# Kernel optimization log

Hardware: AMD Instinct MI355X
Metric: run time of the kernel (lower is better)

The kernel has to match this reference:

```python
import jax, jax.numpy as jnp
import numpy as np

ATTWSIZE = 64  # sliding window length (matches init_kwargs attwsize)


def setup_inputs() -> dict:
    key = jax.random.key(0)
    k1, k2, k3 = jax.random.split(key, 3)
    B, T, D, A = 32, 4096, 256, 128
    x = jax.random.normal(k1, (B, T, D), dtype=jnp.float32)
    Wp = jax.random.normal(k2, (A, D), dtype=jnp.float32) / np.sqrt(D).astype(np.float32)
    bp = jnp.zeros((A,), dtype=jnp.float32)
    Wg = jax.random.normal(k3, (1, A), dtype=jnp.float32) / np.sqrt(A).astype(np.float32)
    return {"x": x, "Wp": Wp, "bp": bp, "Wg": Wg}


def _windowed_sum(v, w):
    # causal sliding-window sum over axis=1: sum(v[:, max(t-w+1,0):t+1, :])
    # single-pass cumsum formulation: cs[t] - cs[t-w]
    cs = jnp.cumsum(v, axis=1)
    T = v.shape[1]
    shifted = jnp.pad(cs, ((0, 0), (w, 0), (0, 0)))[:, :T, :]
    return cs - shifted


def reference(x, Wp, bp, Wg):
    # proj = tanh(Linear(dimio->dimatt)(x))
    proj = jnp.tanh(jnp.einsum('btd,ad->bta', x, Wp) + bp)
    # gvec = sigmoid(Linear(dimatt->1, no bias)(proj))  -> [B, T, 1]
    g = jax.nn.sigmoid(jnp.einsum('bta,oa->bto', proj, Wg))
    wx = g * x  # gated input [B, T, D]
    num = _windowed_sum(wx, ATTWSIZE)         # [B, T, D]
    den = _windowed_sum(g, ATTWSIZE)          # [B, T, 1] broadcasts over D
    return num / den
```

## Files before the change

kernel.cpp:

```cpp
#include <hip/hip_runtime.h>

#define TT 4096
#define DD 256
#define AA 128
#define WIN 64

typedef short bf16x8 __attribute__((ext_vector_type(8)));
typedef float f32x4 __attribute__((ext_vector_type(4)));
typedef unsigned int u32x4 __attribute__((ext_vector_type(4)));

__device__ __forceinline__ unsigned short f2bf(float f) {
    unsigned int u = __builtin_bit_cast(unsigned int, f);
    u += 0x7FFFu + ((u >> 16) & 1u);
    return (unsigned short)(u >> 16);
}

__device__ __forceinline__ unsigned int cvt_pk_bf16(float lo, float hi) {
    unsigned int r;
    asm("v_cvt_pk_bf16_f32 %0, %1, %2" : "=v"(r) : "v"(lo), "v"(hi));
    return r;
}

__global__ __launch_bounds__(256) void prep_wp(const float* __restrict__ Wp,
                                               unsigned short* __restrict__ wpb) {
    int i = blockIdx.x * 256 + threadIdx.x;
    wpb[i] = f2bf(Wp[i]);
}

#define SROWS 32
#define TC    512
#define NU    ((TC + WIN) / SROWS)
#define NCHK  (TT / TC)

__global__ __launch_bounds__(256, 1) void fused_kernel(
        const float* __restrict__ x, const unsigned short* __restrict__ wpb,
        const float* __restrict__ bp, const float* __restrict__ Wg,
        float* __restrict__ out) {
    __shared__ __align__(16) float xs[4][SROWS * DD];
    __shared__ float gbuf[4][SROWS];
    __shared__ float psum[4][SROWS];
    const int tid  = threadIdx.x;
    const int lane = tid & 63;
    const int wave = tid >> 6;
    const int quad = lane >> 4;
    const int nrow = lane & 15;
    const int sw   = nrow & 7;
    const int b     = blockIdx.x >> 3;
    const int chunk = blockIdx.x & (NCHK - 1);
    const long t0   = (long)chunk * TC;
    const float* xb = x   + (size_t)b * TT * DD;
    float*       ob = out + (size_t)b * TT * DD;

    bf16x8 bfrag[2][8];
    float bpv[2], wgv[2];
#pragma unroll
    for (int nt = 0; nt < 2; ++nt) {
        int n = wave * 32 + nt * 16 + nrow;
        bpv[nt] = bp[n];
        wgv[nt] = Wg[n];
#pragma unroll
        for (int k0 = 0; k0 < 8; ++k0)
            bfrag[nt][k0] = *reinterpret_cast<const bf16x8*>(
                wpb + n * DD + k0 * 32 + quad * 8);
    }

    auto stage = [&](int u) {
        const int nb = u & 3;
        const long r0 = t0 - WIN + (long)u * SROWS;
#pragma unroll
        for (int j = 0; j < 8; ++j) {
            int r = wave * 8 + j;
            long row = r0 + r;
            row = row < 0 ? 0 : row;
            const float* gp = xb + row * DD + ((lane ^ (r & 7)) << 2);
            __builtin_amdgcn_global_load_lds(
                (const __attribute__((address_space(1))) void*)gp,
                (__attribute__((address_space(3))) void*)&xs[nb][r * DD],
                16, 0, 0);
        }
    };

    float S = 0.f, Sg = 0.f;

    stage(0);
    asm volatile("s_waitcnt vmcnt(0)" ::: "memory");
    __builtin_amdgcn_sched_barrier(0);
    __builtin_amdgcn_s_barrier();
    __builtin_amdgcn_sched_barrier(0);

    for (int u = 0; u < NU; ++u) {
        if (u + 1 < NU) stage(u + 1);

        const float* buf = xs[u & 3];
        f32x4 acc[2][2];
#pragma unroll
        for (int mt = 0; mt < 2; ++mt)
#pragma unroll
            for (int nt = 0; nt < 2; ++nt)
                acc[mt][nt] = (f32x4){0.f, 0.f, 0.f, 0.f};
#pragma unroll
        for (int k0 = 0; k0 < 8; ++k0) {
#pragma unroll
            for (int mt = 0; mt < 2; ++mt) {
                const float* rowp = buf + (mt * 16 + nrow) * DD;
                const int gidx = quad * 2 + k0 * 8;
                float4 f0 = *reinterpret_cast<const float4*>(rowp + (((gidx)     ^ sw) << 2));
                float4 f1 = *reinterpret_cast<const float4*>(rowp + (((gidx + 1) ^ sw) << 2));
                u32x4 w;
                w.x = cvt_pk_bf16(f0.x, f0.y);
                w.y = cvt_pk_bf16(f0.z, f0.w);
                w.z = cvt_pk_bf16(f1.x, f1.y);
                w.w = cvt_pk_bf16(f1.z, f1.w);
                bf16x8 af = __builtin_bit_cast(bf16x8, w);
                acc[mt][0] = __builtin_amdgcn_mfma_f32_16x16x32_bf16(af, bfrag[0][k0], acc[mt][0], 0, 0, 0);
                acc[mt][1] = __builtin_amdgcn_mfma_f32_16x16x32_bf16(af, bfrag[1][k0], acc[mt][1], 0, 0, 0);
            }
        }
        float p[2][4];
#pragma unroll
        for (int mt = 0; mt < 2; ++mt)
#pragma unroll
            for (int r = 0; r < 4; ++r) p[mt][r] = 0.f;
#pragma unroll
        for (int nt = 0; nt < 2; ++nt) {
#pragma unroll
            for (int mt = 0; mt < 2; ++mt) {
#pragma unroll
                for (int r = 0; r < 4; ++r) {
                    float pre = acc[mt][nt][r] + bpv[nt];
                    float e  = __expf(2.0f * pre);
                    float th = 1.0f - 2.0f * __builtin_amdgcn_rcpf(e + 1.0f);
                    p[mt][r] += th * wgv[nt];
                }
            }
        }
#pragma unroll
        for (int off = 1; off <= 8; off <<= 1)
#pragma unroll
            for (int mt = 0; mt < 2; ++mt)
#pragma unroll
                for (int r = 0; r < 4; ++r)
                    p[mt][r] += __shfl_xor(p[mt][r], off, 64);
        if (nrow == 0) {
#pragma unroll
            for (int mt = 0; mt < 2; ++mt)
#pragma unroll
                for (int r = 0; r < 4; ++r)
                    psum[wave][mt * 16 + quad * 4 + r] = p[mt][r];
        }

        asm volatile("s_waitcnt lgkmcnt(0)" ::: "memory");
        __builtin_amdgcn_sched_barrier(0);
        __builtin_amdgcn_s_barrier();
        __builtin_amdgcn_sched_barrier(0);

        if (tid < SROWS) {
            float ssum = psum[0][tid] + psum[1][tid] + psum[2][tid] + psum[3][tid];
            float gg = __builtin_amdgcn_rcpf(1.0f + __expf(-ssum));
            long row = t0 - WIN + (long)u * SROWS + tid;
            gbuf[u & 3][tid] = (row < 0) ? 0.f : gg;
        }
        asm volatile("s_waitcnt lgkmcnt(0)" ::: "memory");
        __builtin_amdgcn_sched_barrier(0);
        __builtin_amdgcn_s_barrier();
        __builtin_amdgcn_sched_barrier(0);

        if (u >= 2) {
            const int v  = u - 2;
            const int bn = u & 3, bo = v & 3;
            const float* fn = xs[bn];
            const float* fo = xs[bo];
            const long tbase = t0 + (long)v * SROWS;
#pragma unroll 8
            for (int tt = 0; tt < SROWS; ++tt) {
                int off = tt * DD + ((((tid >> 2) ^ (tt & 7)) << 2) | (tid & 3));
                float gnew = gbuf[bn][tt];
                float gold = gbuf[bo][tt];
                S  += gnew * fn[off] - gold * fo[off];
                Sg += gnew - gold;
                ob[(tbase + tt) * DD + tid] = S * __builtin_amdgcn_rcpf(Sg);
            }
        } else {
            const int bn = u & 3;
            const float* fn = xs[bn];
#pragma unroll 8
            for (int tt = 0; tt < SROWS; ++tt) {
                int off = tt * DD + ((((tid >> 2) ^ (tt & 7)) << 2) | (tid & 3));
                float gnew = gbuf[bn][tt];
                S  += gnew * fn[off];
                Sg += gnew;
            }
        }

        asm volatile("s_waitcnt vmcnt(0)" ::: "memory");
        __builtin_amdgcn_sched_barrier(0);
        __builtin_amdgcn_s_barrier();
        __builtin_amdgcn_sched_barrier(0);
    }
}

extern "C" void kernel_launch(void* const* d_in, const int* in_sizes, int n_in,
                              void* d_out, int out_size, void* d_ws, size_t ws_size,
                              hipStream_t stream) {
    const float* x  = (const float*)d_in[0];
    const float* Wp = (const float*)d_in[1];
    const float* bp = (const float*)d_in[2];
    const float* Wg = (const float*)d_in[3];
    float* out = (float*)d_out;

    unsigned short* wpb = (unsigned short*)d_ws;

    prep_wp<<<AA * DD / 256, 256, 0, stream>>>(Wp, wpb);
    fused_kernel<<<32 * NCHK, 256, 0, stream>>>(x, wpb, bp, Wg, out);
}
```

Baseline: 266.3 us.

## Drop LDS staging of x, read directly from global/L2, halve chunk size

Removes the async global-to-LDS staging ring buffer of x. The MFMA projection now loads A fragments straight from global memory, and the windowed-sum loop re-reads the new and old rows of x from global, relying on L2 and cache hits. Chunk length drops from 512 to 256 rows and launch bounds allow two blocks per CU, giving twice as many blocks and more occupancy now that LDS use is small. The cost is that x is read from memory several times per chunk, including the WIN-row halo, which is now a larger share of each shorter chunk. This bets on cache reuse to make up for losing explicit prefetch overlap and one barrier per step.

```diff
diff --git a/kernel.cpp b/kernel.cpp
--- a/kernel.cpp
+++ b/kernel.cpp
@@ -28,15 +28,14 @@
 }
 
 #define SROWS 32
-#define TC    512
+#define TC    256
 #define NU    ((TC + WIN) / SROWS)
 #define NCHK  (TT / TC)
 
-__global__ __launch_bounds__(256, 1) void fused_kernel(
+__global__ __launch_bounds__(256, 2) void fused_kernel(
         const float* __restrict__ x, const unsigned short* __restrict__ wpb,
         const float* __restrict__ bp, const float* __restrict__ Wg,
         float* __restrict__ out) {
-    __shared__ __align__(16) float xs[4][SROWS * DD];
     __shared__ float gbuf[4][SROWS];
     __shared__ float psum[4][SROWS];
     const int tid  = threadIdx.x;
@@ -44,8 +43,7 @@
     const int wave = tid >> 6;
     const int quad = lane >> 4;
     const int nrow = lane & 15;
-    const int sw   = nrow & 7;
-    const int b     = blockIdx.x >> 3;
+    const int b     = blockIdx.x >> 4;
     const int chunk = blockIdx.x & (NCHK - 1);
     const long t0   = (long)chunk * TC;
     const float* xb = x   + (size_t)b * TT * DD;
@@ -64,58 +62,50 @@
                 wpb + n * DD + k0 * 32 + quad * 8);
     }
 
-    auto stage = [&](int u) {
-        const int nb = u & 3;
-        const long r0 = t0 - WIN + (long)u * SROWS;
-#pragma unroll
-        for (int j = 0; j < 8; ++j) {
-            int r = wave * 8 + j;
-            long row = r0 + r;
-            row = row < 0 ? 0 : row;
-            const float* gp = xb + row * DD + ((lane ^ (r & 7)) << 2);
-            __builtin_amdgcn_global_load_lds(
-                (const __attribute__((address_space(1))) void*)gp,
-                (__attribute__((address_space(3))) void*)&xs[nb][r * DD],
-                16, 0, 0);
-        }
-    };
-
     float S = 0.f, Sg = 0.f;
 
-    stage(0);
-    asm volatile("s_waitcnt vmcnt(0)" ::: "memory");
-    __builtin_amdgcn_sched_barrier(0);
-    __builtin_amdgcn_s_barrier();
-    __builtin_amdgcn_sched_barrier(0);
-
     for (int u = 0; u < NU; ++u) {
-        if (u + 1 < NU) stage(u + 1);
-
-        const float* buf = xs[u & 3];
+        const long rbase = t0 - WIN + (long)u * SROWS;
+
+        long R0 = rbase + nrow;
+        long R1 = rbase + 16 + nrow;
+        if (rbase < 0) {
+            R0 = R0 < 0 ? 0 : R0;
+            R1 = R1 < 0 ? 0 : R1;
+        }
+        const float* rp0 = xb + R0 * DD + quad * 8;
+        const float* rp1 = xb + R1 * DD + quad * 8;
+
         f32x4 acc[2][2];
 #pragma unroll
         for (int mt = 0; mt < 2; ++mt)
 #pragma unroll
             for (int nt = 0; nt < 2; ++nt)
                 acc[mt][nt] = (f32x4){0.f, 0.f, 0.f, 0.f};
+
 #pragma unroll
         for (int k0 = 0; k0 < 8; ++k0) {
-#pragma unroll
-            for (int mt = 0; mt < 2; ++mt) {
-                const float* rowp = buf + (mt * 16 + nrow) * DD;
-                const int gidx = quad * 2 + k0 * 8;
-                float4 f0 = *reinterpret_cast<const float4*>(rowp + (((gidx)     ^ sw) << 2));
-                float4 f1 = *reinterpret_cast<const float4*>(rowp + (((gidx + 1) ^ sw) << 2));
-                u32x4 w;
-                w.x = cvt_pk_bf16(f0.x, f0.y);
-                w.y = cvt_pk_bf16(f0.z, f0.w);
-                w.z = cvt_pk_bf16(f1.x, f1.y);
-                w.w = cvt_pk_bf16(f1.z, f1.w);
-                bf16x8 af = __builtin_bit_cast(bf16x8, w);
-                acc[mt][0] = __builtin_amdgcn_mfma_f32_16x16x32_bf16(af, bfrag[0][k0], acc[mt][0], 0, 0, 0);
-                acc[mt][1] = __builtin_amdgcn_mfma_f32_16x16x32_bf16(af, bfrag[1][k0], acc[mt][1], 0, 0, 0);
-            }
-        }
+            float4 a0 = *reinterpret_cast<const float4*>(rp0 + k0 * 32);
+            float4 a1 = *reinterpret_cast<const float4*>(rp0 + k0 * 32 + 4);
+            float4 c0 = *reinterpret_cast<const float4*>(rp1 + k0 * 32);
+            float4 c1 = *reinterpret_cast<const float4*>(rp1 + k0 * 32 + 4);
+            u32x4 w0, w1;
+            w0.x = cvt_pk_bf16(a0.x, a0.y);
+            w0.y = cvt_pk_bf16(a0.z, a0.w);
+            w0.z = cvt_pk_bf16(a1.x, a1.y);
+            w0.w = cvt_pk_bf16(a1.z, a1.w);
+            w1.x = cvt_pk_bf16(c0.x, c0.y);
+            w1.y = cvt_pk_bf16(c0.z, c0.w);
+            w1.z = cvt_pk_bf16(c1.x, c1.y);
+            w1.w = cvt_pk_bf16(c1.z, c1.w);
+            bf16x8 af0 = __builtin_bit_cast(bf16x8, w0);
+            bf16x8 af1 = __builtin_bit_cast(bf16x8, w1);
+            acc[0][0] = __builtin_amdgcn_mfma_f32_16x16x32_bf16(af0, bfrag[0][k0], acc[0][0], 0, 0, 0);
+            acc[0][1] = __builtin_amdgcn_mfma_f32_16x16x32_bf16(af0, bfrag[1][k0], acc[0][1], 0, 0, 0);
+            acc[1][0] = __builtin_amdgcn_mfma_f32_16x16x32_bf16(af1, bfrag[0][k0], acc[1][0], 0, 0, 0);
+            acc[1][1] = __builtin_amdgcn_mfma_f32_16x16x32_bf16(af1, bfrag[1][k0], acc[1][1], 0, 0, 0);
+        }
+
         float p[2][4];
 #pragma unroll
         for (int mt = 0; mt < 2; ++mt)
@@ -157,8 +147,7 @@
         if (tid < SROWS) {
             float ssum = psum[0][tid] + psum[1][tid] + psum[2][tid] + psum[3][tid];
             float gg = __builtin_amdgcn_rcpf(1.0f + __expf(-ssum));
-            long row = t0 - WIN + (long)u * SROWS + tid;
-            gbuf[u & 3][tid] = (row < 0) ? 0.f : gg;
+            gbuf[u & 3][tid] = (rbase + tid < 0) ? 0.f : gg;
         }
         asm volatile("s_waitcnt lgkmcnt(0)" ::: "memory");
         __builtin_amdgcn_sched_barrier(0);
@@ -166,36 +155,33 @@
         __builtin_amdgcn_sched_barrier(0);
 
         if (u >= 2) {
-            const int v  = u - 2;
-            const int bn = u & 3, bo = v & 3;
-            const float* fn = xs[bn];
-            const float* fo = xs[bo];
-            const long tbase = t0 + (long)v * SROWS;
-#pragma unroll 8
+            const float* gn = gbuf[u & 3];
+            const float* go = gbuf[(u + 2) & 3];
+            const long tb = t0 + (long)(u - 2) * SROWS;
+#pragma unroll 16
             for (int tt = 0; tt < SROWS; ++tt) {
-                int off = tt * DD + ((((tid >> 2) ^ (tt & 7)) << 2) | (tid & 3));
-                float gnew = gbuf[bn][tt];
-                float gold = gbuf[bo][tt];
-                S  += gnew * fn[off] - gold * fo[off];
+                long tn = tb + tt;
+                long to = tn - WIN;
+                to = to < 0 ? 0 : to;
+                float gnew = gn[tt];
+                float gold = go[tt];
+                float xn = xb[tn * DD + tid];
+                float xo = xb[to * DD + tid];
+                S  += gnew * xn - gold * xo;
                 Sg += gnew - gold;
-                ob[(tbase + tt) * DD + tid] = S * __builtin_amdgcn_rcpf(Sg);
+                ob[tn * DD + tid] = S * __builtin_amdgcn_rcpf(Sg);
             }
         } else {
-            const int bn = u & 3;
-            const float* fn = xs[bn];
-#pragma unroll 8
+            const float* gn = gbuf[u & 3];
+#pragma unroll 16
             for (int tt = 0; tt < SROWS; ++tt) {
-                int off = tt * DD + ((((tid >> 2) ^ (tt & 7)) << 2) | (tid & 3));
-                float gnew = gbuf[bn][tt];
-                S  += gnew * fn[off];
+                long rn = rbase + tt;
+                rn = rn < 0 ? 0 : rn;
+                float gnew = gn[tt];
+                S  += gnew * xb[rn * DD + tid];
                 Sg += gnew;
             }
         }
-
-        asm volatile("s_waitcnt vmcnt(0)" ::: "memory");
-        __builtin_amdgcn_sched_barrier(0);
-        __builtin_amdgcn_s_barrier();
-        __builtin_amdgcn_sched_barrier(0);
     }
 }
 
```

Measured after the change: 404.1 us. 1.52x slower.

## Halve chunk size, double-buffer LDS, and read scan inputs from global memory

Applied to the files above, without the earlier changes.

Chunk length drops from 512 to 256, giving twice as many blocks, and the LDS staging shrinks from 4 to 2 buffers so two blocks can share a CU (launch bounds 256,2). The windowed-scan stage now lags the gate computation by one step and re-reads x rows straight from global/L2 instead of keeping older tiles in LDS. One barrier per iteration is removed and vmcnt(8) lets the next tile's loads stay in flight. The cost is extra global reads for the new and old rows, plus more warmup overhead because each shorter chunk still recomputes the 64-row halo.

```diff
diff --git a/kernel.cpp b/kernel.cpp
--- a/kernel.cpp
+++ b/kernel.cpp
@@ -28,15 +28,15 @@
 }
 
 #define SROWS 32
-#define TC    512
+#define TC    256
 #define NU    ((TC + WIN) / SROWS)
 #define NCHK  (TT / TC)
 
-__global__ __launch_bounds__(256, 1) void fused_kernel(
+__global__ __launch_bounds__(256, 2) void fused_kernel(
         const float* __restrict__ x, const unsigned short* __restrict__ wpb,
         const float* __restrict__ bp, const float* __restrict__ Wg,
         float* __restrict__ out) {
-    __shared__ __align__(16) float xs[4][SROWS * DD];
+    __shared__ __align__(16) float xs[2][SROWS * DD];
     __shared__ float gbuf[4][SROWS];
     __shared__ float psum[4][SROWS];
     const int tid  = threadIdx.x;
@@ -45,7 +45,7 @@
     const int quad = lane >> 4;
     const int nrow = lane & 15;
     const int sw   = nrow & 7;
-    const int b     = blockIdx.x >> 3;
+    const int b     = blockIdx.x >> 4;
     const int chunk = blockIdx.x & (NCHK - 1);
     const long t0   = (long)chunk * TC;
     const float* xb = x   + (size_t)b * TT * DD;
@@ -64,9 +64,9 @@
                 wpb + n * DD + k0 * 32 + quad * 8);
     }
 
-    auto stage = [&](int u) {
-        const int nb = u & 3;
-        const long r0 = t0 - WIN + (long)u * SROWS;
+    auto stage = [&](int su) {
+        const int nb = su & 1;
+        const long r0 = t0 - WIN + (long)su * SROWS;
 #pragma unroll
         for (int j = 0; j < 8; ++j) {
             int r = wave * 8 + j;
@@ -83,70 +83,74 @@
     float S = 0.f, Sg = 0.f;
 
     stage(0);
-    asm volatile("s_waitcnt vmcnt(0)" ::: "memory");
-    __builtin_amdgcn_sched_barrier(0);
-    __builtin_amdgcn_s_barrier();
-    __builtin_amdgcn_sched_barrier(0);
-
-    for (int u = 0; u < NU; ++u) {
+
+    for (int u = 0; u <= NU; ++u) {
         if (u + 1 < NU) stage(u + 1);
 
-        const float* buf = xs[u & 3];
-        f32x4 acc[2][2];
-#pragma unroll
-        for (int mt = 0; mt < 2; ++mt)
-#pragma unroll
-            for (int nt = 0; nt < 2; ++nt)
-                acc[mt][nt] = (f32x4){0.f, 0.f, 0.f, 0.f};
-#pragma unroll
-        for (int k0 = 0; k0 < 8; ++k0) {
-#pragma unroll
-            for (int mt = 0; mt < 2; ++mt) {
-                const float* rowp = buf + (mt * 16 + nrow) * DD;
-                const int gidx = quad * 2 + k0 * 8;
-                float4 f0 = *reinterpret_cast<const float4*>(rowp + (((gidx)     ^ sw) << 2));
-                float4 f1 = *reinterpret_cast<const float4*>(rowp + (((gidx + 1) ^ sw) << 2));
-                u32x4 w;
-                w.x = cvt_pk_bf16(f0.x, f0.y);
-                w.y = cvt_pk_bf16(f0.z, f0.w);
-                w.z = cvt_pk_bf16(f1.x, f1.y);
-                w.w = cvt_pk_bf16(f1.z, f1.w);
-                bf16x8 af = __builtin_bit_cast(bf16x8, w);
-                acc[mt][0] = __builtin_amdgcn_mfma_f32_16x16x32_bf16(af, bfrag[0][k0], acc[mt][0], 0, 0, 0);
-                acc[mt][1] = __builtin_amdgcn_mfma_f32_16x16x32_bf16(af, bfrag[1][k0], acc[mt][1], 0, 0, 0);
-            }
-        }
-        float p[2][4];
-#pragma unroll
-        for (int mt = 0; mt < 2; ++mt)
-#pragma unroll
-            for (int r = 0; r < 4; ++r) p[mt][r] = 0.f;
-#pragma unroll
-        for (int nt = 0; nt < 2; ++nt) {
-#pragma unroll
-            for (int mt = 0; mt < 2; ++mt) {
-#pragma unroll
-                for (int r = 0; r < 4; ++r) {
-                    float pre = acc[mt][nt][r] + bpv[nt];
-                    float e  = __expf(2.0f * pre);
-                    float th = 1.0f - 2.0f * __builtin_amdgcn_rcpf(e + 1.0f);
-                    p[mt][r] += th * wgv[nt];
-                }
-            }
-        }
-#pragma unroll
-        for (int off = 1; off <= 8; off <<= 1)
+        if (u + 1 < NU) asm volatile("s_waitcnt vmcnt(8) lgkmcnt(0)" ::: "memory");
+        else            asm volatile("s_waitcnt vmcnt(0) lgkmcnt(0)" ::: "memory");
+        __builtin_amdgcn_sched_barrier(0);
+        __builtin_amdgcn_s_barrier();
+        __builtin_amdgcn_sched_barrier(0);
+
+        if (u < NU) {
+            const float* buf = xs[u & 1];
+            f32x4 acc[2][2];
 #pragma unroll
             for (int mt = 0; mt < 2; ++mt)
 #pragma unroll
-                for (int r = 0; r < 4; ++r)
-                    p[mt][r] += __shfl_xor(p[mt][r], off, 64);
-        if (nrow == 0) {
+                for (int nt = 0; nt < 2; ++nt)
+                    acc[mt][nt] = (f32x4){0.f, 0.f, 0.f, 0.f};
+#pragma unroll
+            for (int k0 = 0; k0 < 8; ++k0) {
+#pragma unroll
+                for (int mt = 0; mt < 2; ++mt) {
+                    const float* rowp = buf + (mt * 16 + nrow) * DD;
+                    const int gidx = quad * 2 + k0 * 8;
+                    float4 f0 = *reinterpret_cast<const float4*>(rowp + (((gidx)     ^ sw) << 2));
+                    float4 f1 = *reinterpret_cast<const float4*>(rowp + (((gidx + 1) ^ sw) << 2));
+                    u32x4 w;
+                    w.x = cvt_pk_bf16(f0.x, f0.y);
+                    w.y = cvt_pk_bf16(f0.z, f0.w);
+                    w.z = cvt_pk_bf16(f1.x, f1.y);
+                    w.w = cvt_pk_bf16(f1.z, f1.w);
+                    bf16x8 af = __builtin_bit_cast(bf16x8, w);
+                    acc[mt][0] = __builtin_amdgcn_mfma_f32_16x16x32_bf16(af, bfrag[0][k0], acc[mt][0], 0, 0, 0);
+                    acc[mt][1] = __builtin_amdgcn_mfma_f32_16x16x32_bf16(af, bfrag[1][k0], acc[mt][1], 0, 0, 0);
+                }
+            }
+            float p[2][4];
 #pragma unroll
             for (int mt = 0; mt < 2; ++mt)
 #pragma unroll
-                for (int r = 0; r < 4; ++r)
-                    psum[wave][mt * 16 + quad * 4 + r] = p[mt][r];
+                for (int r = 0; r < 4; ++r) p[mt][r] = 0.f;
+#pragma unroll
+            for (int nt = 0; nt < 2; ++nt) {
+#pragma unroll
+                for (int mt = 0; mt < 2; ++mt) {
+#pragma unroll
+                    for (int r = 0; r < 4; ++r) {
+                        float pre = acc[mt][nt][r] + bpv[nt];
+                        float e  = __expf(2.0f * pre);
+                        float th = 1.0f - 2.0f * __builtin_amdgcn_rcpf(e + 1.0f);
+                        p[mt][r] += th * wgv[nt];
+                    }
+                }
+            }
+#pragma unroll
+            for (int off = 1; off <= 8; off <<= 1)
+#pragma unroll
+                for (int mt = 0; mt < 2; ++mt)
+#pragma unroll
+                    for (int r = 0; r < 4; ++r)
+                        p[mt][r] += __shfl_xor(p[mt][r], off, 64);
+            if (nrow == 0) {
+#pragma unroll
+                for (int mt = 0; mt < 2; ++mt)
+#pragma unroll
+                    for (int r = 0; r < 4; ++r)
+                        psum[wave][mt * 16 + quad * 4 + r] = p[mt][r];
+            }
         }
 
         asm volatile("s_waitcnt lgkmcnt(0)" ::: "memory");
@@ -154,48 +158,43 @@
         __builtin_amdgcn_s_barrier();
         __builtin_amdgcn_sched_barrier(0);
 
-        if (tid < SROWS) {
+        if (u < NU && tid < SROWS) {
             float ssum = psum[0][tid] + psum[1][tid] + psum[2][tid] + psum[3][tid];
             float gg = __builtin_amdgcn_rcpf(1.0f + __expf(-ssum));
             long row = t0 - WIN + (long)u * SROWS + tid;
             gbuf[u & 3][tid] = (row < 0) ? 0.f : gg;
         }
-        asm volatile("s_waitcnt lgkmcnt(0)" ::: "memory");
-        __builtin_amdgcn_sched_barrier(0);
-        __builtin_amdgcn_s_barrier();
-        __builtin_amdgcn_sched_barrier(0);
-
-        if (u >= 2) {
-            const int v  = u - 2;
-            const int bn = u & 3, bo = v & 3;
-            const float* fn = xs[bn];
-            const float* fo = xs[bo];
-            const long tbase = t0 + (long)v * SROWS;
-#pragma unroll 8
-            for (int tt = 0; tt < SROWS; ++tt) {
-                int off = tt * DD + ((((tid >> 2) ^ (tt & 7)) << 2) | (tid & 3));
-                float gnew = gbuf[bn][tt];
-                float gold = gbuf[bo][tt];
-                S  += gnew * fn[off] - gold * fo[off];
-                Sg += gnew - gold;
-                ob[(tbase + tt) * DD + tid] = S * __builtin_amdgcn_rcpf(Sg);
-            }
-        } else {
-            const int bn = u & 3;
-            const float* fn = xs[bn];
-#pragma unroll 8
-            for (int tt = 0; tt < SROWS; ++tt) {
-                int off = tt * DD + ((((tid >> 2) ^ (tt & 7)) << 2) | (tid & 3));
-                float gnew = gbuf[bn][tt];
-                S  += gnew * fn[off];
-                Sg += gnew;
-            }
-        }
-
-        asm volatile("s_waitcnt vmcnt(0)" ::: "memory");
-        __builtin_amdgcn_sched_barrier(0);
-        __builtin_amdgcn_s_barrier();
-        __builtin_amdgcn_sched_barrier(0);
+
+        if (u >= 1) {
+            const int w = u - 1;
+            const float* gn = gbuf[w & 3];
+            const long rb = t0 - WIN + (long)w * SROWS;
+            if (w >= 2) {
+                const float* go = gbuf[(w + 2) & 3];
+#pragma unroll 16
+                for (int tt = 0; tt < SROWS; ++tt) {
+                    long tn = rb + tt;
+                    long to = tn - WIN;
+                    to = to < 0 ? 0 : to;
+                    float gnew = gn[tt];
+                    float gold = go[tt];
+                    float xn = xb[tn * DD + tid];
+                    float xo = xb[to * DD + tid];
+                    S  += gnew * xn - gold * xo;
+                    Sg += gnew - gold;
+                    ob[tn * DD + tid] = S * __builtin_amdgcn_rcpf(Sg);
+                }
+            } else {
+#pragma unroll 16
+                for (int tt = 0; tt < SROWS; ++tt) {
+                    long rn = rb + tt;
+                    rn = rn < 0 ? 0 : rn;
+                    float gnew = gn[tt];
+                    S  += gnew * xb[rn * DD + tid];
+                    Sg += gnew;
+                }
+            }
+        }
     }
 }
 
```

Result: no change. 270.7 us (+1.7%).
